# Kernel optimization log

Measured on AMD Instinct MI355X. Metric: run time of the kernel, lower is better.

## Reference

```python
import jax, jax.numpy as jnp
import numpy as np

N_NODES = 100000
N_EDGES = 1600000
IN_CH = 64
OUT_CH = 32
HEADS = 4
NEG_SLOPE = 0.2


def setup_inputs() -> dict:
    key = jax.random.key(0)
    k = jax.random.split(key, 6)
    x = jax.random.normal(k[0], (N_NODES, IN_CH), dtype=jnp.float32)
    edge_index = jax.random.randint(k[1], (2, N_EDGES), 0, N_NODES, dtype=jnp.int32)
    W = jax.random.normal(k[2], (IN_CH, HEADS * OUT_CH), dtype=jnp.float32) * 0.1
    att_src = jax.random.normal(k[3], (1, HEADS, OUT_CH), dtype=jnp.float32) * 0.1
    att_dst = jax.random.normal(k[4], (1, HEADS, OUT_CH), dtype=jnp.float32) * 0.1
    bias = jnp.zeros((HEADS * OUT_CH,), dtype=jnp.float32)
    return {"x": x, "edge_index": edge_index, "W": W,
            "att_src": att_src, "att_dst": att_dst, "bias": bias}


def reference(x, edge_index, W, att_src, att_dst, bias):
    N = x.shape[0]
    H, C = att_src.shape[1], att_src.shape[2]
    # GATConv defaults: add self loops
    loop = jnp.arange(N, dtype=edge_index.dtype)
    src = jnp.concatenate([edge_index[0], loop])  # [E+N]
    dst = jnp.concatenate([edge_index[1], loop])  # [E+N]
    # linear transform -> [N, H, C]
    h = (x @ W).reshape(N, H, C)
    # per-node attention halves: [N, H]
    a_src = jnp.sum(h * att_src, axis=-1)
    a_dst = jnp.sum(h * att_dst, axis=-1)
    # edge scores with LeakyReLU: [E+N, H]
    e = jax.nn.leaky_relu(a_src[src] + a_dst[dst], negative_slope=NEG_SLOPE)
    # segment softmax over destination nodes (numerically stable)
    m = jax.ops.segment_max(e, dst, num_segments=N)           # [N, H]
    m = jnp.where(jnp.isfinite(m), m, 0.0)
    ex = jnp.exp(e - m[dst])                                   # [E+N, H]
    denom = jax.ops.segment_sum(ex, dst, num_segments=N)      # [N, H]
    alpha = ex / (denom[dst] + 1e-16)                          # [E+N, H]
    # scatter-aggregate weighted source features -> [N, H, C]
    out = jax.ops.segment_sum(h[src] * alpha[:, :, None], dst, num_segments=N)
    out = out.reshape(N, H * C) + bias
    return jax.nn.log_softmax(out, axis=1)
```

## Files before the change

### kernel.cpp

```cpp
#include <hip/hip_runtime.h>
#include <hip/hip_bf16.h>

#define IN_CH 64
#define HC 128
#define NHEAD 4
#define NEG 0.2f
#define CAPB 32
#define BWID 128
#define NB 782
#define CAP2 2560
#define CH1 4096
#define VPT 8

typedef short s16x8 __attribute__((ext_vector_type(8)));
typedef float f32x4 __attribute__((ext_vector_type(4)));

__device__ __forceinline__ float leaky(float v) { return fmaxf(v, NEG * v); }
__device__ __forceinline__ unsigned short f2bf(float f) {
    unsigned int u = __float_as_uint(f);
    u += 0x7fff + ((u >> 16) & 1);
    return (unsigned short)(u >> 16);
}
__device__ __forceinline__ float4 add4(float4 a, float4 b) {
    return make_float4(a.x + b.x, a.y + b.y, a.z + b.z, a.w + b.w);
}
__device__ __forceinline__ float4 leaky4(float4 v) {
    return make_float4(leaky(v.x), leaky(v.y), leaky(v.z), leaky(v.w));
}
__device__ __forceinline__ float4 exp4(float4 v) {
    return make_float4(__expf(v.x), __expf(v.y), __expf(v.z), __expf(v.w));
}
__device__ __forceinline__ float comp4(float4 v, int i) {
    float r = v.x;
    r = (i == 1) ? v.y : r;
    r = (i == 2) ? v.z : r;
    r = (i == 3) ? v.w : r;
    return r;
}

#define ACC8(al, hv)                                                  \
    do {                                                              \
        acc[0] = fmaf((al), __uint_as_float((hv).x << 16), acc[0]);   \
        acc[1] = fmaf((al), __uint_as_float((hv).x & 0xffff0000u), acc[1]); \
        acc[2] = fmaf((al), __uint_as_float((hv).y << 16), acc[2]);   \
        acc[3] = fmaf((al), __uint_as_float((hv).y & 0xffff0000u), acc[3]); \
        acc[4] = fmaf((al), __uint_as_float((hv).z << 16), acc[4]);   \
        acc[5] = fmaf((al), __uint_as_float((hv).z & 0xffff0000u), acc[5]); \
        acc[6] = fmaf((al), __uint_as_float((hv).w << 16), acc[6]);   \
        acc[7] = fmaf((al), __uint_as_float((hv).w & 0xffff0000u), acc[7]); \
    } while (0)

__global__ void __launch_bounds__(256) k_prep(
        const float* __restrict__ W, const float* __restrict__ att_src,
        const float* __restrict__ att_dst, unsigned short* __restrict__ wtp,
        int* __restrict__ bcnt) {
    const int t = threadIdx.x;
    for (int i = t; i < NB * 16; i += 256) bcnt[i] = 0;
    for (int idx = t; idx < 144 * 64; idx += 256) {
        const int c = idx >> 6, k = idx & 63;
        float v = 0.f;
        if (c < HC) v = W[k * HC + c];
        else if (c < HC + 8) {
            const int j = c - HC, h = j & 3;
            const float* att = (j < 4) ? att_src : att_dst;
#pragma unroll
            for (int cc = 0; cc < 32; ++cc)
                v += W[k * HC + h * 32 + cc] * att[h * 32 + cc];
        }
        wtp[c * 72 + k] = f2bf(v);
    }
    for (int idx = t; idx < 144 * 8; idx += 256)
        wtp[(idx >> 3) * 72 + 64 + (idx & 7)] = 0;
}

__global__ void __launch_bounds__(512, 2) k_front(
        const float* __restrict__ x, const unsigned short* __restrict__ wtp,
        unsigned short* __restrict__ h_bf, float* __restrict__ a_src,
        float* __restrict__ a_dst,
        const int* __restrict__ src, const int* __restrict__ dst,
        int* __restrict__ bcnt, int* __restrict__ pairs,
        int E, int N, int NXB) {
    __shared__ union {
        struct { unsigned short xs[128][72]; unsigned short wt[144][72]; } xf;
        struct { int hist[NB]; int scanbuf[1024]; int startb[NB]; int gbase[NB];
                 int lbuf[CH1]; int gposb[CH1]; } bn;
    } sm;
    const int t = threadIdx.x;
    const int r3 = blockIdx.x % 3;

    if (r3 < 2) {
        const int xb = (blockIdx.x / 3) * 2 + r3;
        if (xb >= NXB) return;
        const int rowbase_blk = xb * 128;

        for (int idx = t; idx < 1296; idx += 512)
            ((uint4*)sm.xf.wt)[idx] = ((const uint4*)wtp)[idx];
        for (int idx = t; idx < (128 * IN_CH) / 4; idx += 512) {
            const int row = idx >> 4;
            const int c0 = (idx & 15) * 4;
            const int grow = min(rowbase_blk + row, N - 1);
            const float4 v = ((const float4*)(x + (size_t)grow * IN_CH))[idx & 15];
            const unsigned int p0 = (unsigned int)f2bf(v.x) | ((unsigned int)f2bf(v.y) << 16);
            const unsigned int p1 = (unsigned int)f2bf(v.z) | ((unsigned int)f2bf(v.w) << 16);
            *(uint2*)&sm.xf.xs[row][c0] = make_uint2(p0, p1);
        }
        __syncthreads();

        const int lane = t & 63;
        const int w = t >> 6;
        const int rbase = w * 16;
        const int lr = lane & 15, lq = lane >> 4;

        f32x4 acc[9];
#pragma unroll
        for (int n = 0; n < 9; ++n) acc[n] = (f32x4){0.f, 0.f, 0.f, 0.f};

#pragma unroll
        for (int ks = 0; ks < 2; ++ks) {
            const s16x8 a0 = *(const s16x8*)&sm.xf.xs[rbase + lr][ks * 32 + lq * 8];
#pragma unroll
            for (int n = 0; n < 9; ++n) {
                const s16x8 b = *(const s16x8*)&sm.xf.wt[n * 16 + lr][ks * 32 + lq * 8];
                acc[n] = __builtin_amdgcn_mfma_f32_16x16x32_bf16(a0, b, acc[n], 0, 0, 0);
            }
        }

#pragma unroll
        for (int j = 0; j < 4; ++j) {
            const int grow = rowbase_blk + rbase + lq * 4 + j;
            if (grow >= N) continue;
#pragma unroll
            for (int n = 0; n < 8; ++n)
                h_bf[(size_t)grow * HC + n * 16 + lr] = f2bf(acc[n][j]);
            const float av = acc[8][j];
            if (lr < 4) a_src[grow * NHEAD + lr] = av;
            else if (lr < 8) a_dst[grow * NHEAD + (lr - 4)] = av;
        }
    } else {
        const int bb = blockIdx.x / 3;
        const int base = bb * CH1;
        const int cnt = min(CH1, E - base);

        for (int i = t; i < NB; i += 512) sm.bn.hist[i] = 0;
        __syncthreads();

        int pk[VPT]; int rb[VPT];
#pragma unroll
        for (int k = 0; k < VPT; ++k) {
            const int idx = base + k * 512 + t;
            if (idx < E) {
                const int s = src[idx], d = dst[idx];
                const int b = d >> 7;
                const int dl = d & 127;
                pk[k] = (dl << 17) | s;
                const int rank = atomicAdd(&sm.bn.hist[b], 1);
                rb[k] = (b << 16) | rank;
            } else {
                pk[k] = 0; rb[k] = -1;
            }
        }
        __syncthreads();

        sm.bn.scanbuf[t] = (t < NB) ? sm.bn.hist[t] : 0;
        sm.bn.scanbuf[t + 512] = (t + 512 < NB) ? sm.bn.hist[t + 512] : 0;
        __syncthreads();
        for (int off = 1; off < 1024; off <<= 1) {
            const int a0 = (t >= off) ? sm.bn.scanbuf[t - off] : 0;
            const int a1 = (t + 512 >= off) ? sm.bn.scanbuf[t + 512 - off] : 0;
            __syncthreads();
            sm.bn.scanbuf[t] += a0;
            sm.bn.scanbuf[t + 512] += a1;
            __syncthreads();
        }
        for (int i = t; i < NB; i += 512) {
            const int h = sm.bn.hist[i];
            sm.bn.startb[i] = sm.bn.scanbuf[i] - h;
            sm.bn.gbase[i] = (h > 0) ? atomicAdd(&bcnt[i * 16], h) : 0;
        }
        __syncthreads();

#pragma unroll
        for (int k = 0; k < VPT; ++k) {
            if (rb[k] >= 0) {
                const int b = rb[k] >> 16;
                const int rank = rb[k] & 0xffff;
                const int lpos = sm.bn.startb[b] + rank;
                const int gp = sm.bn.gbase[b] + rank;
                sm.bn.lbuf[lpos] = pk[k];
                sm.bn.gposb[lpos] = (gp < CAP2) ? (b * CAP2 + gp) : -1;
            }
        }
        __syncthreads();

        for (int i = t; i < cnt; i += 512) {
            const int g = sm.bn.gposb[i];
            if (g >= 0) pairs[g] = sm.bn.lbuf[i];
        }
    }
}

__global__ void __launch_bounds__(256) k_fill(
        const int* __restrict__ bcnt, const int* __restrict__ pairs,
        int* __restrict__ srcbuf, int* __restrict__ rowstart,
        int* __restrict__ deg, int N) {
    const int b = blockIdx.x;
    const int t = threadIdx.x;
    __shared__ int scnt[BWID];
    __shared__ int cur[BWID];
    __shared__ int scan2[256];
    __shared__ int slist[CAP2];
    __shared__ int sbase_s;

    int part = 0;
    for (int i = t; i < b; i += 256) part += min(bcnt[i * 16], CAP2);
    scan2[t] = part; __syncthreads();
    for (int off = 128; off > 0; off >>= 1) {
        if (t < off) scan2[t] += scan2[t + off];
        __syncthreads();
    }
    if (t == 0) sbase_s = scan2[0];
    if (t < BWID) scnt[t] = 0;
    __syncthreads();

    const int mc = min(bcnt[b * 16], CAP2);
    const int pb = b * CAP2;

    for (int i = t; i < mc; i += 256)
        atomicAdd(&scnt[pairs[pb + i] >> 17], 1);
    __syncthreads();

    if (t < BWID) scan2[t] = scnt[t];
    __syncthreads();
    for (int off = 1; off < BWID; off <<= 1) {
        const int add = (t >= off && t < BWID) ? scan2[t - off] : 0;
        __syncthreads();
        if (t < BWID) scan2[t] += add;
        __syncthreads();
    }
    if (t < BWID) {
        const int ex = scan2[t] - scnt[t];
        cur[t] = ex;
        const int n = b * BWID + t;
        if (n < N) {
            rowstart[n] = sbase_s + ex;
            deg[n] = scnt[t];
        }
    }
    __syncthreads();

    for (int i = t; i < mc; i += 256) {
        const int e = pairs[pb + i];
        const int p = atomicAdd(&cur[e >> 17], 1);
        slist[p] = e & 0x1ffff;
    }
    __syncthreads();

    for (int i = t; i < mc; i += 256) srcbuf[sbase_s + i] = slist[i];
}

__global__ void __launch_bounds__(256) k_node(
        const int* __restrict__ deg_, const int* __restrict__ rowstart,
        const int* __restrict__ srcbuf,
        const float* __restrict__ a_src, const float* __restrict__ a_dst,
        const unsigned short* __restrict__ h_bf, const float* __restrict__ bias,
        float* __restrict__ out, int N) {
    const int slot = threadIdx.x >> 4;
    const int l = threadIdx.x & 15;
    int n = blockIdx.x * 16 + slot;
    n = min(n, N - 1);
    const int deg = deg_[n];
    const int start = rowstart[n];
    const int dcap = min(deg, CAPB);

    __shared__ float s_ex[16][CAPB + 1][NHEAD];
    __shared__ int   s_src[16][CAPB + 1];

    const float4 ad4  = *(const float4*)(a_dst + n * NHEAD);
    const float4 asn4 = *(const float4*)(a_src + n * NHEAD);

    float4 sum4 = make_float4(0.f, 0.f, 0.f, 0.f);
    for (int j = l; j < dcap; j += 16) {
        const int s = srcbuf[start + j];
        s_src[slot][j] = s;
        const float4 a = *(const float4*)(a_src + s * NHEAD);
        const float4 e4 = exp4(leaky4(add4(a, ad4)));
        *(float4*)&s_ex[slot][j][0] = e4;
        sum4 = add4(sum4, e4);
    }
    for (int j = CAPB + l; j < deg; j += 16) {
        const int s = srcbuf[start + j];
        const float4 a = *(const float4*)(a_src + s * NHEAD);
        sum4 = add4(sum4, exp4(leaky4(add4(a, ad4))));
    }
#pragma unroll
    for (int off = 1; off < 16; off <<= 1) {
        sum4.x += __shfl_xor(sum4.x, off, 64);
        sum4.y += __shfl_xor(sum4.y, off, 64);
        sum4.z += __shfl_xor(sum4.z, off, 64);
        sum4.w += __shfl_xor(sum4.w, off, 64);
    }
    const float4 self4 = exp4(leaky4(add4(asn4, ad4)));
    sum4 = add4(sum4, self4);
    const float4 r4v = make_float4(1.f / (sum4.x + 1e-16f), 1.f / (sum4.y + 1e-16f),
                                   1.f / (sum4.z + 1e-16f), 1.f / (sum4.w + 1e-16f));

    __builtin_amdgcn_wave_barrier();

    const int hd = l >> 2;
    const float rsel = comp4(r4v, hd);
    const float adh  = comp4(ad4, hd);
    float acc[8];
#pragma unroll
    for (int k = 0; k < 8; ++k) acc[k] = 0.f;

    int j = 0;
    for (; j + 8 <= dcap; j += 8) {
        const int s0 = s_src[slot][j];
        const int s1 = s_src[slot][j + 1];
        const int s2 = s_src[slot][j + 2];
        const int s3 = s_src[slot][j + 3];
        const int s4 = s_src[slot][j + 4];
        const int s5 = s_src[slot][j + 5];
        const int s6 = s_src[slot][j + 6];
        const int s7 = s_src[slot][j + 7];
        const uint4 h0 = *(const uint4*)(h_bf + (size_t)s0 * HC + l * 8);
        const uint4 h1 = *(const uint4*)(h_bf + (size_t)s1 * HC + l * 8);
        const uint4 h2 = *(const uint4*)(h_bf + (size_t)s2 * HC + l * 8);
        const uint4 h3 = *(const uint4*)(h_bf + (size_t)s3 * HC + l * 8);
        const uint4 h4 = *(const uint4*)(h_bf + (size_t)s4 * HC + l * 8);
        const uint4 h5 = *(const uint4*)(h_bf + (size_t)s5 * HC + l * 8);
        const uint4 h6 = *(const uint4*)(h_bf + (size_t)s6 * HC + l * 8);
        const uint4 h7 = *(const uint4*)(h_bf + (size_t)s7 * HC + l * 8);
        const float al0 = s_ex[slot][j][hd];
        const float al1 = s_ex[slot][j + 1][hd];
        const float al2 = s_ex[slot][j + 2][hd];
        const float al3 = s_ex[slot][j + 3][hd];
        const float al4 = s_ex[slot][j + 4][hd];
        const float al5 = s_ex[slot][j + 5][hd];
        const float al6 = s_ex[slot][j + 6][hd];
        const float al7 = s_ex[slot][j + 7][hd];
        ACC8(al0, h0); ACC8(al1, h1); ACC8(al2, h2); ACC8(al3, h3);
        ACC8(al4, h4); ACC8(al5, h5); ACC8(al6, h6); ACC8(al7, h7);
    }
    for (; j + 2 <= dcap; j += 2) {
        const int s0 = s_src[slot][j];
        const int s1 = s_src[slot][j + 1];
        const uint4 h0 = *(const uint4*)(h_bf + (size_t)s0 * HC + l * 8);
        const uint4 h1 = *(const uint4*)(h_bf + (size_t)s1 * HC + l * 8);
        const float al0 = s_ex[slot][j][hd];
        const float al1 = s_ex[slot][j + 1][hd];
        ACC8(al0, h0);
        ACC8(al1, h1);
    }
    if (j < dcap) {
        const int s0 = s_src[slot][j];
        const uint4 h0 = *(const uint4*)(h_bf + (size_t)s0 * HC + l * 8);
        const float al0 = s_ex[slot][j][hd];
        ACC8(al0, h0);
    }
    for (int jj = CAPB; jj < deg; ++jj) {
        const int s = srcbuf[start + jj];
        const float al = __expf(leaky(a_src[s * NHEAD + hd] + adh));
        const uint4 hv = *(const uint4*)(h_bf + (size_t)s * HC + l * 8);
        ACC8(al, hv);
    }
    {
        const float als = comp4(self4, hd);
        const uint4 hv = *(const uint4*)(h_bf + (size_t)n * HC + l * 8);
        ACC8(als, hv);
    }

    const float4 b0 = *(const float4*)(bias + l * 8);
    const float4 b1 = *(const float4*)(bias + l * 8 + 4);
    acc[0] = acc[0] * rsel + b0.x; acc[1] = acc[1] * rsel + b0.y;
    acc[2] = acc[2] * rsel + b0.z; acc[3] = acc[3] * rsel + b0.w;
    acc[4] = acc[4] * rsel + b1.x; acc[5] = acc[5] * rsel + b1.y;
    acc[6] = acc[6] * rsel + b1.z; acc[7] = acc[7] * rsel + b1.w;

    float mxv = fmaxf(fmaxf(fmaxf(acc[0], acc[1]), fmaxf(acc[2], acc[3])),
                      fmaxf(fmaxf(acc[4], acc[5]), fmaxf(acc[6], acc[7])));
#pragma unroll
    for (int off = 1; off < 16; off <<= 1) mxv = fmaxf(mxv, __shfl_xor(mxv, off, 64));
    float se = 0.f;
#pragma unroll
    for (int k = 0; k < 8; ++k) se += __expf(acc[k] - mxv);
#pragma unroll
    for (int off = 1; off < 16; off <<= 1) se += __shfl_xor(se, off, 64);
    const float lse = mxv + __logf(se);

    float* op = out + (size_t)n * HC + l * 8;
    *(float4*)op = make_float4(acc[0] - lse, acc[1] - lse, acc[2] - lse, acc[3] - lse);
    *(float4*)(op + 4) = make_float4(acc[4] - lse, acc[5] - lse, acc[6] - lse, acc[7] - lse);
}

extern "C" void kernel_launch(void* const* d_in, const int* in_sizes, int n_in,
                              void* d_out, int out_size, void* d_ws, size_t ws_size,
                              hipStream_t stream) {
    const float* x       = (const float*)d_in[0];
    const int*   ei      = (const int*)d_in[1];
    const float* W       = (const float*)d_in[2];
    const float* att_src = (const float*)d_in[3];
    const float* att_dst = (const float*)d_in[4];
    const float* bias    = (const float*)d_in[5];
    float* out = (float*)d_out;

    const int N = in_sizes[0] / IN_CH;
    const int E = in_sizes[1] / 2;
    const int* src = ei;
    const int* dst = ei + E;

    char* wsb = (char*)d_ws;
    unsigned short* h_bf = (unsigned short*)wsb;    wsb += (size_t)N * HC * 2;
    float* a_src  = (float*)wsb;                    wsb += (size_t)N * NHEAD * 4;
    float* a_dst  = (float*)wsb;                    wsb += (size_t)N * NHEAD * 4;
    int*   bcnt   = (int*)wsb;                      wsb += (size_t)NB * 16 * 4;
    int*   pairs  = (int*)wsb;                      wsb += (size_t)NB * CAP2 * 4;
    int*   srcbuf = (int*)wsb;                      wsb += (size_t)E * 4;
    int*   rowstart = (int*)wsb;                    wsb += (size_t)N * 4;
    int*   deg    = (int*)wsb;                      wsb += (size_t)N * 4;
    unsigned short* wtp = (unsigned short*)wsb;     wsb += 144 * 72 * 2;

    const int NXB = (N + 127) / 128;
    const int NBB = (E + CH1 - 1) / CH1;

    k_prep<<<1, 256, 0, stream>>>(W, att_src, att_dst, wtp, bcnt);
    k_front<<<NBB * 3, 512, 0, stream>>>(x, wtp, h_bf, a_src, a_dst,
                                         src, dst, bcnt, pairs, E, N, NXB);
    k_fill<<<NB, 256, 0, stream>>>(bcnt, pairs, srcbuf, rowstart, deg, N);
    k_node<<<(N + 15) / 16, 256, 0, stream>>>(deg, rowstart, srcbuf,
                                              a_src, a_dst,
                                              (const unsigned short*)h_bf, bias, out, N);
}
```

Before: 219.4 us.

## Split fused front kernel into separate transform and binning kernels

Splits the combined k_front kernel, which alternated GEMM blocks and edge-binning blocks, into two separate launches, k_xform and k_bin, each with its own shared memory. The GEMM now swaps the MFMA operands so each lane holds four consecutive output columns, which allows packed 8-byte bf16 stores and float4 stores for the attention halves instead of scalar stores. It also removes the 8-way unrolled gather loop in k_node, leaving the 2-way loop. The split adds a launch and removes overlap between the two independent phases, and the smaller unroll lowers memory-level parallelism in the gather while reducing register pressure.

After: 224.6 us. 2.4% more time.

```diff
diff --git a/kernel.cpp b/kernel.cpp
--- a/kernel.cpp
+++ b/kernel.cpp
@@ -73,129 +73,133 @@
         wtp[(idx >> 3) * 72 + 64 + (idx & 7)] = 0;
 }
 
-__global__ void __launch_bounds__(512, 2) k_front(
+__global__ void __launch_bounds__(512, 2) k_xform(
         const float* __restrict__ x, const unsigned short* __restrict__ wtp,
         unsigned short* __restrict__ h_bf, float* __restrict__ a_src,
-        float* __restrict__ a_dst,
+        float* __restrict__ a_dst, int N) {
+    __shared__ unsigned short xs[128][72];
+    __shared__ unsigned short wt[144][72];
+    const int t = threadIdx.x;
+    const int rowbase_blk = blockIdx.x * 128;
+
+    for (int idx = t; idx < 1296; idx += 512)
+        ((uint4*)wt)[idx] = ((const uint4*)wtp)[idx];
+    for (int idx = t; idx < (128 * IN_CH) / 4; idx += 512) {
+        const int row = idx >> 4;
+        const int c0 = (idx & 15) * 4;
+        const int grow = min(rowbase_blk + row, N - 1);
+        const float4 v = ((const float4*)(x + (size_t)grow * IN_CH))[idx & 15];
+        const unsigned int p0 = (unsigned int)f2bf(v.x) | ((unsigned int)f2bf(v.y) << 16);
+        const unsigned int p1 = (unsigned int)f2bf(v.z) | ((unsigned int)f2bf(v.w) << 16);
+        *(uint2*)&xs[row][c0] = make_uint2(p0, p1);
+    }
+    __syncthreads();
+
+    const int lane = t & 63;
+    const int w = t >> 6;
+    const int rbase = w * 16;
+    const int lr = lane & 15, lq = lane >> 4;
+
+    f32x4 acc[9];
+#pragma unroll
+    for (int n = 0; n < 9; ++n) acc[n] = (f32x4){0.f, 0.f, 0.f, 0.f};
+
+#pragma unroll
+    for (int ks = 0; ks < 2; ++ks) {
+        const s16x8 xb = *(const s16x8*)&xs[rbase + lr][ks * 32 + lq * 8];
+#pragma unroll
+        for (int n = 0; n < 9; ++n) {
+            const s16x8 wa = *(const s16x8*)&wt[n * 16 + lr][ks * 32 + lq * 8];
+            acc[n] = __builtin_amdgcn_mfma_f32_16x16x32_bf16(wa, xb, acc[n], 0, 0, 0);
+        }
+    }
+
+    const int node = rowbase_blk + rbase + lr;
+    if (node < N) {
+#pragma unroll
+        for (int n = 0; n < 8; ++n) {
+            const unsigned int p0 = (unsigned int)f2bf(acc[n][0]) |
+                                    ((unsigned int)f2bf(acc[n][1]) << 16);
+            const unsigned int p1 = (unsigned int)f2bf(acc[n][2]) |
+                                    ((unsigned int)f2bf(acc[n][3]) << 16);
+            *(uint2*)(h_bf + (size_t)node * HC + n * 16 + lq * 4) = make_uint2(p0, p1);
+        }
+        if (lq == 0)
+            *(float4*)(a_src + node * NHEAD) =
+                make_float4(acc[8][0], acc[8][1], acc[8][2], acc[8][3]);
+        else if (lq == 1)
+            *(float4*)(a_dst + node * NHEAD) =
+                make_float4(acc[8][0], acc[8][1], acc[8][2], acc[8][3]);
+    }
+}
+
+__global__ void __launch_bounds__(512, 2) k_bin(
         const int* __restrict__ src, const int* __restrict__ dst,
-        int* __restrict__ bcnt, int* __restrict__ pairs,
-        int E, int N, int NXB) {
-    __shared__ union {
-        struct { unsigned short xs[128][72]; unsigned short wt[144][72]; } xf;
-        struct { int hist[NB]; int scanbuf[1024]; int startb[NB]; int gbase[NB];
-                 int lbuf[CH1]; int gposb[CH1]; } bn;
-    } sm;
+        int* __restrict__ bcnt, int* __restrict__ pairs, int E) {
+    __shared__ int hist[NB];
+    __shared__ int scanbuf[1024];
+    __shared__ int startb[NB];
+    __shared__ int gbase[NB];
+    __shared__ int lbuf[CH1];
+    __shared__ int gposb[CH1];
     const int t = threadIdx.x;
-    const int r3 = blockIdx.x % 3;
-
-    if (r3 < 2) {
-        const int xb = (blockIdx.x / 3) * 2 + r3;
-        if (xb >= NXB) return;
-        const int rowbase_blk = xb * 128;
-
-        for (int idx = t; idx < 1296; idx += 512)
-            ((uint4*)sm.xf.wt)[idx] = ((const uint4*)wtp)[idx];
-        for (int idx = t; idx < (128 * IN_CH) / 4; idx += 512) {
-            const int row = idx >> 4;
-            const int c0 = (idx & 15) * 4;
-            const int grow = min(rowbase_blk + row, N - 1);
-            const float4 v = ((const float4*)(x + (size_t)grow * IN_CH))[idx & 15];
-            const unsigned int p0 = (unsigned int)f2bf(v.x) | ((unsigned int)f2bf(v.y) << 16);
-            const unsigned int p1 = (unsigned int)f2bf(v.z) | ((unsigned int)f2bf(v.w) << 16);
-            *(uint2*)&sm.xf.xs[row][c0] = make_uint2(p0, p1);
-        }
+    const int base = blockIdx.x * CH1;
+    const int cnt = min(CH1, E - base);
+
+    for (int i = t; i < NB; i += 512) hist[i] = 0;
+    __syncthreads();
+
+    int pk[VPT]; int rb[VPT];
+#pragma unroll
+    for (int k = 0; k < VPT; ++k) {
+        const int idx = base + k * 512 + t;
+        if (idx < E) {
+            const int s = src[idx], d = dst[idx];
+            const int b = d >> 7;
+            const int dl = d & 127;
+            pk[k] = (dl << 17) | s;
+            const int rank = atomicAdd(&hist[b], 1);
+            rb[k] = (b << 16) | rank;
+        } else {
+            pk[k] = 0; rb[k] = -1;
+        }
+    }
+    __syncthreads();
+
+    scanbuf[t] = (t < NB) ? hist[t] : 0;
+    scanbuf[t + 512] = (t + 512 < NB) ? hist[t + 512] : 0;
+    __syncthreads();
+    for (int off = 1; off < 1024; off <<= 1) {
+        const int a0 = (t >= off) ? scanbuf[t - off] : 0;
+        const int a1 = (t + 512 >= off) ? scanbuf[t + 512 - off] : 0;
         __syncthreads();
-
-        const int lane = t & 63;
-        const int w = t >> 6;
-        const int rbase = w * 16;
-        const int lr = lane & 15, lq = lane >> 4;
-
-        f32x4 acc[9];
-#pragma unroll
-        for (int n = 0; n < 9; ++n) acc[n] = (f32x4){0.f, 0.f, 0.f, 0.f};
-
-#pragma unroll
-        for (int ks = 0; ks < 2; ++ks) {
-            const s16x8 a0 = *(const s16x8*)&sm.xf.xs[rbase + lr][ks * 32 + lq * 8];
-#pragma unroll
-            for (int n = 0; n < 9; ++n) {
-                const s16x8 b = *(const s16x8*)&sm.xf.wt[n * 16 + lr][ks * 32 + lq * 8];
-                acc[n] = __builtin_amdgcn_mfma_f32_16x16x32_bf16(a0, b, acc[n], 0, 0, 0);
-            }
-        }
-
-#pragma unroll
-        for (int j = 0; j < 4; ++j) {
-            const int grow = rowbase_blk + rbase + lq * 4 + j;
-            if (grow >= N) continue;
-#pragma unroll
-            for (int n = 0; n < 8; ++n)
-                h_bf[(size_t)grow * HC + n * 16 + lr] = f2bf(acc[n][j]);
-            const float av = acc[8][j];
-            if (lr < 4) a_src[grow * NHEAD + lr] = av;
-            else if (lr < 8) a_dst[grow * NHEAD + (lr - 4)] = av;
-        }
-    } else {
-        const int bb = blockIdx.x / 3;
-        const int base = bb * CH1;
-        const int cnt = min(CH1, E - base);
-
-        for (int i = t; i < NB; i += 512) sm.bn.hist[i] = 0;
+        scanbuf[t] += a0;
+        scanbuf[t + 512] += a1;
         __syncthreads();
-
-        int pk[VPT]; int rb[VPT];
-#pragma unroll
-        for (int k = 0; k < VPT; ++k) {
-            const int idx = base + k * 512 + t;
-            if (idx < E) {
-                const int s = src[idx], d = dst[idx];
-                const int b = d >> 7;
-                const int dl = d & 127;
-                pk[k] = (dl << 17) | s;
-                const int rank = atomicAdd(&sm.bn.hist[b], 1);
-                rb[k] = (b << 16) | rank;
-            } else {
-                pk[k] = 0; rb[k] = -1;
-            }
-        }
-        __syncthreads();
-
-        sm.bn.scanbuf[t] = (t < NB) ? sm.bn.hist[t] : 0;
-        sm.bn.scanbuf[t + 512] = (t + 512 < NB) ? sm.bn.hist[t + 512] : 0;
-        __syncthreads();
-        for (int off = 1; off < 1024; off <<= 1) {
-            const int a0 = (t >= off) ? sm.bn.scanbuf[t - off] : 0;
-            const int a1 = (t + 512 >= off) ? sm.bn.scanbuf[t + 512 - off] : 0;
-            __syncthreads();
-            sm.bn.scanbuf[t] += a0;
-            sm.bn.scanbuf[t + 512] += a1;
-            __syncthreads();
-        }
-        for (int i = t; i < NB; i += 512) {
-            const int h = sm.bn.hist[i];
-            sm.bn.startb[i] = sm.bn.scanbuf[i] - h;
-            sm.bn.gbase[i] = (h > 0) ? atomicAdd(&bcnt[i * 16], h) : 0;
-        }
-        __syncthreads();
-
-#pragma unroll
-        for (int k = 0; k < VPT; ++k) {
-            if (rb[k] >= 0) {
-                const int b = rb[k] >> 16;
-                const int rank = rb[k] & 0xffff;
-                const int lpos = sm.bn.startb[b] + rank;
-                const int gp = sm.bn.gbase[b] + rank;
-                sm.bn.lbuf[lpos] = pk[k];
-                sm.bn.gposb[lpos] = (gp < CAP2) ? (b * CAP2 + gp) : -1;
-            }
-        }
-        __syncthreads();
-
-        for (int i = t; i < cnt; i += 512) {
-            const int g = sm.bn.gposb[i];
-            if (g >= 0) pairs[g] = sm.bn.lbuf[i];
-        }
+    }
+    for (int i = t; i < NB; i += 512) {
+        const int h = hist[i];
+        startb[i] = scanbuf[i] - h;
+        gbase[i] = (h > 0) ? atomicAdd(&bcnt[i * 16], h) : 0;
+    }
+    __syncthreads();
+
+#pragma unroll
+    for (int k = 0; k < VPT; ++k) {
+        if (rb[k] >= 0) {
+            const int b = rb[k] >> 16;
+            const int rank = rb[k] & 0xffff;
+            const int lpos = startb[b] + rank;
+            const int gp = gbase[b] + rank;
+            lbuf[lpos] = pk[k];
+            gposb[lpos] = (gp < CAP2) ? (b * CAP2 + gp) : -1;
+        }
+    }
+    __syncthreads();
+
+    for (int i = t; i < cnt; i += 512) {
+        const int g = gposb[i];
+        if (g >= 0) pairs[g] = lbuf[i];
     }
 }
 
@@ -314,34 +318,6 @@
     for (int k = 0; k < 8; ++k) acc[k] = 0.f;
 
     int j = 0;
-    for (; j + 8 <= dcap; j += 8) {
-        const int s0 = s_src[slot][j];
-        const int s1 = s_src[slot][j + 1];
-        const int s2 = s_src[slot][j + 2];
-        const int s3 = s_src[slot][j + 3];
-        const int s4 = s_src[slot][j + 4];
-        const int s5 = s_src[slot][j + 5];
-        const int s6 = s_src[slot][j + 6];
-        const int s7 = s_src[slot][j + 7];
-        const uint4 h0 = *(const uint4*)(h_bf + (size_t)s0 * HC + l * 8);
-        const uint4 h1 = *(const uint4*)(h_bf + (size_t)s1 * HC + l * 8);
-        const uint4 h2 = *(const uint4*)(h_bf + (size_t)s2 * HC + l * 8);
-        const uint4 h3 = *(const uint4*)(h_bf + (size_t)s3 * HC + l * 8);
-        const uint4 h4 = *(const uint4*)(h_bf + (size_t)s4 * HC + l * 8);
-        const uint4 h5 = *(const uint4*)(h_bf + (size_t)s5 * HC + l * 8);
-        const uint4 h6 = *(const uint4*)(h_bf + (size_t)s6 * HC + l * 8);
-        const uint4 h7 = *(const uint4*)(h_bf + (size_t)s7 * HC + l * 8);
-        const float al0 = s_ex[slot][j][hd];
-        const float al1 = s_ex[slot][j + 1][hd];
-        const float al2 = s_ex[slot][j + 2][hd];
-        const float al3 = s_ex[slot][j + 3][hd];
-        const float al4 = s_ex[slot][j + 4][hd];
-        const float al5 = s_ex[slot][j + 5][hd];
-        const float al6 = s_ex[slot][j + 6][hd];
-        const float al7 = s_ex[slot][j + 7][hd];
-        ACC8(al0, h0); ACC8(al1, h1); ACC8(al2, h2); ACC8(al3, h3);
-        ACC8(al4, h4); ACC8(al5, h5); ACC8(al6, h6); ACC8(al7, h7);
-    }
     for (; j + 2 <= dcap; j += 2) {
         const int s0 = s_src[slot][j];
         const int s1 = s_src[slot][j + 1];
@@ -424,8 +400,8 @@
     const int NBB = (E + CH1 - 1) / CH1;
 
     k_prep<<<1, 256, 0, stream>>>(W, att_src, att_dst, wtp, bcnt);
-    k_front<<<NBB * 3, 512, 0, stream>>>(x, wtp, h_bf, a_src, a_dst,
-                                         src, dst, bcnt, pairs, E, N, NXB);
+    k_xform<<<NXB, 512, 0, stream>>>(x, wtp, h_bf, a_src, a_dst, N);
+    k_bin<<<NBB, 512, 0, stream>>>(src, dst, bcnt, pairs, E);
     k_fill<<<NB, 256, 0, stream>>>(bcnt, pairs, srcbuf, rowstart, deg, N);
     k_node<<<(N + 15) / 16, 256, 0, stream>>>(deg, rowstart, srcbuf,
                                               a_src, a_dst,
```
